# Kernel optimization log

Measured on AMD Instinct MI355X. Metric: run time of the kernel, lower is better.

The kernel has to match this reference:

```python
import jax, jax.numpy as jnp
import numpy as np

B, T, DE, DD, A, FN, FS = 32, 2000, 512, 1024, 128, 32, 16
TEMPERATURE = 1.0


def setup_inputs() -> dict:
    key = jax.random.key(0)
    ks = jax.random.split(key, 10)
    input_enc = jax.random.normal(ks[0], (B, T, DE), dtype=jnp.float32)
    # lengths in [T//2, T] so no zero-length utterances
    enc_lengths = jax.random.randint(ks[1], (B,), T // 2, T + 1, dtype=jnp.int32)
    input_dec = jax.random.normal(ks[2], (B, DD), dtype=jnp.float32)
    # prev_att: previous-step attention weights (masked, normalized)
    prev_att = jax.random.uniform(ks[3], (B, T), dtype=jnp.float32)
    pad = jnp.arange(T)[None, :] >= enc_lengths[:, None]
    prev_att = jnp.where(pad, 0.0, prev_att)
    prev_att = prev_att / jnp.sum(prev_att, axis=1, keepdims=True)
    # parameters
    conv_w = jax.random.normal(ks[4], (FN, 1, 2 * FS + 1), dtype=jnp.float32) * 0.1  # [out,in,k]
    enc_w = jax.random.normal(ks[5], (A, DE), dtype=jnp.float32) * 0.04
    dec_w = jax.random.normal(ks[6], (A, DD), dtype=jnp.float32) * 0.03
    att_w = jax.random.normal(ks[7], (A, FN), dtype=jnp.float32) * 0.17
    att_b = jnp.zeros((A,), dtype=jnp.float32)
    out_w = jax.random.normal(ks[8], (1, A), dtype=jnp.float32) * 0.09
    return dict(input_enc=input_enc, enc_lengths=enc_lengths, input_dec=input_dec,
                prev_att=prev_att, conv_w=conv_w, enc_w=enc_w, dec_w=dec_w,
                att_w=att_w, att_b=att_b, out_w=out_w)


def reference(input_enc, enc_lengths, input_dec, prev_att,
              conv_w, enc_w, dec_w, att_w, att_b, out_w):
    b, t, _ = input_enc.shape
    fs = (conv_w.shape[-1] - 1) // 2  # 'same' padding
    # padding mask: True at padded positions t >= length
    mask = jnp.arange(t)[None, :] >= enc_lengths[:, None]  # [B,T]
    # location features: Conv1d over prev attention, 1 -> FN channels, same length
    conv = jax.lax.conv_general_dilated(
        prev_att[:, None, :], conv_w, window_strides=(1,),
        padding=[(fs, fs)], dimension_numbers=("NCH", "OIH", "NCH"))  # [B,FN,T]
    loc_feat = conv.transpose(0, 2, 1)  # [B,T,FN]
    projected_att = loc_feat @ att_w.T + att_b        # [B,T,A]
    projected_enc = input_enc @ enc_w.T               # [B,T,A]
    projected_dec = (input_dec @ dec_w.T)[:, None, :]  # [B,1,A]
    score = jnp.squeeze(jnp.tanh(projected_att + projected_enc + projected_dec) @ out_w.T, -1)  # [B,T]
    score = jnp.where(mask, -jnp.inf, score)
    att_weight = jax.nn.softmax(TEMPERATURE * score, axis=1)  # [B,T]
    context = jnp.einsum("btd,bt->bd", input_enc, att_weight)  # [B,DE]
    return context, att_weight
```

## Files before the change

### kernel.cpp

```cpp
#include <hip/hip_runtime.h>
#include <hip/hip_bf16.h>
#include <math.h>

#define B_ 32
#define T_ 2000
#define DE_ 512
#define DD_ 1024
#define A_ 128
#define FN_ 32
#define FS_ 16
#define KW_ (2*FS_+1)

typedef __bf16 bf16x8 __attribute__((ext_vector_type(8)));
typedef __bf16 bf16x4 __attribute__((ext_vector_type(4)));
typedef float f32x4 __attribute__((ext_vector_type(4)));

#define BT 64
#define LSTR 40

__global__ __launch_bounds__(256) void cvt_kernel(
    const float* __restrict__ enc_w, const float* __restrict__ att_w,
    __bf16* __restrict__ enc_bf, __bf16* __restrict__ att_bf)
{
    int i = blockIdx.x * 256 + threadIdx.x;
    float4 v = ((const float4*)enc_w)[i];
    bf16x4 o;
    o[0] = (__bf16)v.x; o[1] = (__bf16)v.y; o[2] = (__bf16)v.z; o[3] = (__bf16)v.w;
    *(bf16x4*)(enc_bf + (size_t)i * 4) = o;
    if (i < (A_ * FN_) / 4) {
        float4 w = ((const float4*)att_w)[i];
        bf16x4 p;
        p[0] = (__bf16)w.x; p[1] = (__bf16)w.y; p[2] = (__bf16)w.z; p[3] = (__bf16)w.w;
        *(bf16x4*)(att_bf + (size_t)i * 4) = p;
    }
}

__global__ __launch_bounds__(256) void pdec_kernel(
    const float* __restrict__ input_dec, const float* __restrict__ dec_w,
    const float* __restrict__ att_b, float* __restrict__ pdec)
{
    int b  = blockIdx.y;
    int a0 = blockIdx.x * 32;
    int tid = threadIdx.x;
    int al = tid >> 3;
    int kg = tid & 7;
    int a  = a0 + al;
    const float4* w = (const float4*)(dec_w + (size_t)a * DD_);
    const float4* x = (const float4*)(input_dec + (size_t)b * DD_);
    float acc = 0.f;
    #pragma unroll 8
    for (int j = 0; j < 32; j++) {
        int i4 = kg + j * 8;
        float4 wv = w[i4], xv = x[i4];
        acc += wv.x * xv.x + wv.y * xv.y + wv.z * xv.z + wv.w * xv.w;
    }
    acc += __shfl_xor(acc, 1, 64);
    acc += __shfl_xor(acc, 2, 64);
    acc += __shfl_xor(acc, 4, 64);
    if (kg == 0) pdec[b * A_ + a] = acc + att_b[a];
}

__global__ __launch_bounds__(256, 4) void score_kernel(
    const float* __restrict__ input_enc, const __bf16* __restrict__ enc_bf,
    const float* __restrict__ prev_att,  const float* __restrict__ conv_w,
    const __bf16* __restrict__ att_bf,   const float* __restrict__ pdec,
    const float* __restrict__ out_w,     float* __restrict__ score)
{
    __shared__ float pa_s[BT + 2 * FS_];
    __shared__ float cw_s[KW_ * FN_];
    __shared__ __bf16 loc_s[BT * LSTR];

    const int tid = threadIdx.x;
    const int b  = blockIdx.y;
    const int t0 = blockIdx.x * BT;

    for (int j = tid; j < BT + 2 * FS_; j += 256) {
        int t = t0 - FS_ + j;
        pa_s[j] = (t >= 0 && t < T_) ? prev_att[b * T_ + t] : 0.f;
    }
    for (int idx = tid; idx < FN_ * KW_; idx += 256) {
        int f = idx / KW_, k = idx % KW_;
        cw_s[k * FN_ + f] = conv_w[idx];
    }
    __syncthreads();

    {
        int f = tid & 31, r0 = tid >> 5;
        for (int r = r0; r < BT; r += 8) {
            float acc = 0.f;
            #pragma unroll
            for (int k = 0; k < KW_; k++) acc += pa_s[r + k] * cw_s[k * FN_ + f];
            loc_s[r * LSTR + f] = (__bf16)acc;
        }
    }
    __syncthreads();

    const int lane = tid & 63;
    const int wv   = tid >> 6;
    const int col  = lane & 15;
    const int grp  = lane >> 4;
    const int rowb = wv * 16 + col;
    const int t_row = t0 + rowb;
    const int t_clamp = t_row < T_ ? t_row : T_ - 1;

    f32x4 acc[8];
    const f32x4 zero = (f32x4){0.f, 0.f, 0.f, 0.f};

    {
        bf16x8 afrag = *(const bf16x8*)(loc_s + rowb * LSTR + grp * 8);
        #pragma unroll
        for (int i = 0; i < 8; i++) {
            bf16x8 bfrag = *(const bf16x8*)(att_bf + (size_t)(i * 16 + col) * FN_ + grp * 8);
            acc[i] = __builtin_amdgcn_mfma_f32_16x16x32_bf16(afrag, bfrag, zero, 0, 0, 0);
        }
    }

    const float* arow = input_enc + ((size_t)(b * T_ + t_clamp)) * DE_ + grp * 8;
    const __bf16* bbase = enc_bf + (size_t)col * DE_ + grp * 8;
    #pragma unroll 2
    for (int kc = 0; kc < DE_; kc += 32) {
        float4 a0v = *(const float4*)(arow + kc);
        float4 a1v = *(const float4*)(arow + kc + 4);
        bf16x8 afrag;
        afrag[0] = (__bf16)a0v.x; afrag[1] = (__bf16)a0v.y;
        afrag[2] = (__bf16)a0v.z; afrag[3] = (__bf16)a0v.w;
        afrag[4] = (__bf16)a1v.x; afrag[5] = (__bf16)a1v.y;
        afrag[6] = (__bf16)a1v.z; afrag[7] = (__bf16)a1v.w;
        #pragma unroll
        for (int i = 0; i < 8; i++) {
            bf16x8 bfrag = *(const bf16x8*)(bbase + (size_t)i * 16 * DE_ + kc);
            acc[i] = __builtin_amdgcn_mfma_f32_16x16x32_bf16(afrag, bfrag, acc[i], 0, 0, 0);
        }
    }

    float s[4] = {0.f, 0.f, 0.f, 0.f};
    #pragma unroll
    for (int i = 0; i < 8; i++) {
        int a = i * 16 + col;
        float ow = out_w[a];
        float bias = pdec[b * A_ + a];
        #pragma unroll
        for (int r = 0; r < 4; r++) {
            float v = acc[i][r] + bias;
            v = fminf(fmaxf(v, -15.f), 15.f);
            float e = __expf(2.f * v);
            s[r] += ow * ((e - 1.f) / (e + 1.f));
        }
    }
    #pragma unroll
    for (int r = 0; r < 4; r++) {
        s[r] += __shfl_xor(s[r], 1, 64);
        s[r] += __shfl_xor(s[r], 2, 64);
        s[r] += __shfl_xor(s[r], 4, 64);
        s[r] += __shfl_xor(s[r], 8, 64);
    }
    if (col == 0) {
        #pragma unroll
        for (int r = 0; r < 4; r++) {
            int t = t0 + wv * 16 + grp * 4 + r;
            if (t < T_) score[b * T_ + t] = s[r];
        }
    }
}

__global__ __launch_bounds__(256) void softmax_kernel(
    const float* __restrict__ score, const int* __restrict__ lengths,
    float* __restrict__ att)
{
    int b = blockIdx.x;
    int tid = threadIdx.x;
    int len = lengths[b];
    __shared__ float redm[4], reds[4];

    float m = -1e30f;
    for (int t = tid; t < T_; t += 256)
        if (t < len) m = fmaxf(m, score[b * T_ + t]);
    #pragma unroll
    for (int off = 1; off < 64; off <<= 1) m = fmaxf(m, __shfl_xor(m, off, 64));
    if ((tid & 63) == 0) redm[tid >> 6] = m;
    __syncthreads();
    m = fmaxf(fmaxf(redm[0], redm[1]), fmaxf(redm[2], redm[3]));

    float sum = 0.f;
    for (int t = tid; t < T_; t += 256)
        if (t < len) sum += expf(score[b * T_ + t] - m);
    #pragma unroll
    for (int off = 1; off < 64; off <<= 1) sum += __shfl_xor(sum, off, 64);
    if ((tid & 63) == 0) reds[tid >> 6] = sum;
    __syncthreads();
    sum = reds[0] + reds[1] + reds[2] + reds[3];
    float inv = 1.f / sum;

    for (int t = tid; t < T_; t += 256) {
        float w = (t < len) ? expf(score[b * T_ + t] - m) * inv : 0.f;
        att[b * T_ + t] = w;
    }
}

#define CT 125
__global__ __launch_bounds__(256) void context_kernel(
    const float* __restrict__ enc, const float* __restrict__ att,
    const int* __restrict__ lengths, float* __restrict__ ctx)
{
    int b = blockIdx.y;
    int tstart = blockIdx.x * CT;
    int len = lengths[b];
    int tend = tstart + CT < len ? tstart + CT : len;
    __shared__ float w_s[CT];
    for (int j = threadIdx.x; j < CT; j += 256) w_s[j] = att[b * T_ + tstart + j];
    __syncthreads();
    if (tstart >= tend) return;

    int d0 = threadIdx.x * 2;
    const float* base = enc + ((size_t)(b * T_ + tstart)) * DE_ + d0;
    float ax = 0.f, ay = 0.f;
    int n = tend - tstart;
    #pragma unroll 4
    for (int t = 0; t < n; t++) {
        float w = w_s[t];
        float2 v = *(const float2*)(base + (size_t)t * DE_);
        ax += w * v.x;
        ay += w * v.y;
    }
    atomicAdd(&ctx[b * DE_ + d0], ax);
    atomicAdd(&ctx[b * DE_ + d0 + 1], ay);
}

extern "C" void kernel_launch(void* const* d_in, const int* in_sizes, int n_in,
                              void* d_out, int out_size, void* d_ws, size_t ws_size,
                              hipStream_t stream)
{
    const float* input_enc   = (const float*)d_in[0];
    const int*   enc_lengths = (const int*)d_in[1];
    const float* input_dec   = (const float*)d_in[2];
    const float* prev_att    = (const float*)d_in[3];
    const float* conv_w      = (const float*)d_in[4];
    const float* enc_w       = (const float*)d_in[5];
    const float* dec_w       = (const float*)d_in[6];
    const float* att_w       = (const float*)d_in[7];
    const float* att_b       = (const float*)d_in[8];
    const float* out_w       = (const float*)d_in[9];

    float* out = (float*)d_out;
    char* ws = (char*)d_ws;
    float*  pdec   = (float*)ws;
    float*  score  = (float*)(ws + 16384);
    __bf16* enc_bf = (__bf16*)(ws + 16384 + 256000);
    __bf16* att_bf = (__bf16*)(ws + 16384 + 256000 + 131072);

    hipMemsetAsync(d_out, 0, (size_t)B_ * DE_ * sizeof(float), stream);

    cvt_kernel<<<(A_ * DE_) / 4 / 256, 256, 0, stream>>>(enc_w, att_w, enc_bf, att_bf);

    dim3 pgrid(4, B_);
    pdec_kernel<<<pgrid, 256, 0, stream>>>(input_dec, dec_w, att_b, pdec);

    dim3 sgrid((T_ + BT - 1) / BT, B_);
    score_kernel<<<sgrid, 256, 0, stream>>>(input_enc, enc_bf, prev_att, conv_w,
                                            att_bf, pdec, out_w, score);

    softmax_kernel<<<B_, 256, 0, stream>>>(score, enc_lengths, out + B_ * DE_);

    dim3 cgrid(16, B_);
    context_kernel<<<cgrid, 256, 0, stream>>>(input_enc, out + B_ * DE_, enc_lengths, out);
}
```

Baseline: 276.6 us.

## Stage enc weights in LDS, merge prep kernels, fuse softmax normalize into context

Merges the weight-conversion and decoder-projection kernels into one launch and drops the memset by zeroing the context output inside the softmax-stats kernel. The score kernel now stages bf16 encoder-weight tiles into swizzled shared memory through global_load_lds, instead of each wave reading them from global. Softmax now only computes the max and inverse sum; the context kernel computes the normalized weights, writes them out, and uses float4 loads over more, smaller chunks. This removes launches and a full pass over the scores, at the cost of extra barriers in the score loop and the reuse of the pdec buffer for the softmax stats.

```diff
diff --git a/kernel.cpp b/kernel.cpp
--- a/kernel.cpp
+++ b/kernel.cpp
@@ -18,46 +18,53 @@
 #define BT 64
 #define LSTR 40
 
-__global__ __launch_bounds__(256) void cvt_kernel(
+__device__ __forceinline__ void load_lds16(const void* g, void* l) {
+    __builtin_amdgcn_global_load_lds(
+        (const __attribute__((address_space(1))) unsigned int*)g,
+        (__attribute__((address_space(3))) unsigned int*)l, 16, 0, 0);
+}
+
+__global__ __launch_bounds__(256) void prep_kernel(
     const float* __restrict__ enc_w, const float* __restrict__ att_w,
-    __bf16* __restrict__ enc_bf, __bf16* __restrict__ att_bf)
-{
-    int i = blockIdx.x * 256 + threadIdx.x;
-    float4 v = ((const float4*)enc_w)[i];
-    bf16x4 o;
-    o[0] = (__bf16)v.x; o[1] = (__bf16)v.y; o[2] = (__bf16)v.z; o[3] = (__bf16)v.w;
-    *(bf16x4*)(enc_bf + (size_t)i * 4) = o;
-    if (i < (A_ * FN_) / 4) {
-        float4 w = ((const float4*)att_w)[i];
-        bf16x4 p;
-        p[0] = (__bf16)w.x; p[1] = (__bf16)w.y; p[2] = (__bf16)w.z; p[3] = (__bf16)w.w;
-        *(bf16x4*)(att_bf + (size_t)i * 4) = p;
-    }
-}
-
-__global__ __launch_bounds__(256) void pdec_kernel(
     const float* __restrict__ input_dec, const float* __restrict__ dec_w,
-    const float* __restrict__ att_b, float* __restrict__ pdec)
-{
-    int b  = blockIdx.y;
-    int a0 = blockIdx.x * 32;
-    int tid = threadIdx.x;
-    int al = tid >> 3;
-    int kg = tid & 7;
-    int a  = a0 + al;
-    const float4* w = (const float4*)(dec_w + (size_t)a * DD_);
-    const float4* x = (const float4*)(input_dec + (size_t)b * DD_);
-    float acc = 0.f;
-    #pragma unroll 8
-    for (int j = 0; j < 32; j++) {
-        int i4 = kg + j * 8;
-        float4 wv = w[i4], xv = x[i4];
-        acc += wv.x * xv.x + wv.y * xv.y + wv.z * xv.z + wv.w * xv.w;
-    }
-    acc += __shfl_xor(acc, 1, 64);
-    acc += __shfl_xor(acc, 2, 64);
-    acc += __shfl_xor(acc, 4, 64);
-    if (kg == 0) pdec[b * A_ + a] = acc + att_b[a];
+    const float* __restrict__ att_b,
+    __bf16* __restrict__ enc_bf, __bf16* __restrict__ att_bf,
+    float* __restrict__ pdec)
+{
+    int bx = blockIdx.x, tid = threadIdx.x;
+    if (bx < 64) {
+        int i = bx * 256 + tid;
+        float4 v = ((const float4*)enc_w)[i];
+        bf16x4 o;
+        o[0] = (__bf16)v.x; o[1] = (__bf16)v.y; o[2] = (__bf16)v.z; o[3] = (__bf16)v.w;
+        *(bf16x4*)(enc_bf + (size_t)i * 4) = o;
+        if (i < (A_ * FN_) / 4) {
+            float4 w = ((const float4*)att_w)[i];
+            bf16x4 p;
+            p[0] = (__bf16)w.x; p[1] = (__bf16)w.y; p[2] = (__bf16)w.z; p[3] = (__bf16)w.w;
+            *(bf16x4*)(att_bf + (size_t)i * 4) = p;
+        }
+    } else {
+        int pb = bx - 64;
+        int b  = pb >> 2;
+        int a0 = (pb & 3) * 32;
+        int al = tid >> 3;
+        int kg = tid & 7;
+        int a  = a0 + al;
+        const float4* w = (const float4*)(dec_w + (size_t)a * DD_);
+        const float4* x = (const float4*)(input_dec + (size_t)b * DD_);
+        float acc = 0.f;
+        #pragma unroll 8
+        for (int j = 0; j < 32; j++) {
+            int i4 = kg + j * 8;
+            float4 wv = w[i4], xv = x[i4];
+            acc += wv.x * xv.x + wv.y * xv.y + wv.z * xv.z + wv.w * xv.w;
+        }
+        acc += __shfl_xor(acc, 1, 64);
+        acc += __shfl_xor(acc, 2, 64);
+        acc += __shfl_xor(acc, 4, 64);
+        if (kg == 0) pdec[b * A_ + a] = acc + att_b[a];
+    }
 }
 
 __global__ __launch_bounds__(256, 4) void score_kernel(
@@ -66,9 +73,10 @@
     const __bf16* __restrict__ att_bf,   const float* __restrict__ pdec,
     const float* __restrict__ out_w,     float* __restrict__ score)
 {
+    __shared__ __align__(16) char Bt[16384];
     __shared__ float pa_s[BT + 2 * FS_];
     __shared__ float cw_s[KW_ * FN_];
-    __shared__ __bf16 loc_s[BT * LSTR];
+    __shared__ __align__(16) __bf16 loc_s[BT * LSTR];
 
     const int tid = threadIdx.x;
     const int b  = blockIdx.y;
@@ -102,6 +110,7 @@
     const int rowb = wv * 16 + col;
     const int t_row = t0 + rowb;
     const int t_clamp = t_row < T_ ? t_row : T_ - 1;
+    const int sw = (col & 7);
 
     f32x4 acc[8];
     const f32x4 zero = (f32x4){0.f, 0.f, 0.f, 0.f};
@@ -116,21 +125,43 @@
     }
 
     const float* arow = input_enc + ((size_t)(b * T_ + t_clamp)) * DE_ + grp * 8;
-    const __bf16* bbase = enc_bf + (size_t)col * DE_ + grp * 8;
-    #pragma unroll 2
-    for (int kc = 0; kc < DE_; kc += 32) {
-        float4 a0v = *(const float4*)(arow + kc);
-        float4 a1v = *(const float4*)(arow + kc + 4);
-        bf16x8 afrag;
-        afrag[0] = (__bf16)a0v.x; afrag[1] = (__bf16)a0v.y;
-        afrag[2] = (__bf16)a0v.z; afrag[3] = (__bf16)a0v.w;
-        afrag[4] = (__bf16)a1v.x; afrag[5] = (__bf16)a1v.y;
-        afrag[6] = (__bf16)a1v.z; afrag[7] = (__bf16)a1v.w;
+
+    for (int kc = 0; kc < DE_; kc += 64) {
+        #pragma unroll
+        for (int j = 0; j < 4; j++) {
+            int s  = j * 256 + tid;
+            int r  = s >> 3;
+            int cp = s & 7;
+            int c  = cp ^ (r & 7);
+            load_lds16(enc_bf + (size_t)r * DE_ + kc + c * 8,
+                       Bt + j * 4096 + wv * 1024);
+        }
+        float4 a00 = *(const float4*)(arow + kc);
+        float4 a01 = *(const float4*)(arow + kc + 4);
+        float4 a10 = *(const float4*)(arow + kc + 32);
+        float4 a11 = *(const float4*)(arow + kc + 36);
+        __syncthreads();
+
+        bf16x8 af;
+        af[0] = (__bf16)a00.x; af[1] = (__bf16)a00.y;
+        af[2] = (__bf16)a00.z; af[3] = (__bf16)a00.w;
+        af[4] = (__bf16)a01.x; af[5] = (__bf16)a01.y;
+        af[6] = (__bf16)a01.z; af[7] = (__bf16)a01.w;
         #pragma unroll
         for (int i = 0; i < 8; i++) {
-            bf16x8 bfrag = *(const bf16x8*)(bbase + (size_t)i * 16 * DE_ + kc);
-            acc[i] = __builtin_amdgcn_mfma_f32_16x16x32_bf16(afrag, bfrag, acc[i], 0, 0, 0);
-        }
+            bf16x8 bfrag = *(const bf16x8*)(Bt + (i * 16 + col) * 128 + ((grp ^ sw) * 16));
+            acc[i] = __builtin_amdgcn_mfma_f32_16x16x32_bf16(af, bfrag, acc[i], 0, 0, 0);
+        }
+        af[0] = (__bf16)a10.x; af[1] = (__bf16)a10.y;
+        af[2] = (__bf16)a10.z; af[3] = (__bf16)a10.w;
+        af[4] = (__bf16)a11.x; af[5] = (__bf16)a11.y;
+        af[6] = (__bf16)a11.z; af[7] = (__bf16)a11.w;
+        #pragma unroll
+        for (int i = 0; i < 8; i++) {
+            bf16x8 bfrag = *(const bf16x8*)(Bt + (i * 16 + col) * 128 + (((4 + grp) ^ sw) * 16));
+            acc[i] = __builtin_amdgcn_mfma_f32_16x16x32_bf16(af, bfrag, acc[i], 0, 0, 0);
+        }
+        __syncthreads();
     }
 
     float s[4] = {0.f, 0.f, 0.f, 0.f};
@@ -163,12 +194,14 @@
     }
 }
 
-__global__ __launch_bounds__(256) void softmax_kernel(
+__global__ __launch_bounds__(256) void smax_kernel(
     const float* __restrict__ score, const int* __restrict__ lengths,
-    float* __restrict__ att)
+    float* __restrict__ minv, float* __restrict__ ctx)
 {
     int b = blockIdx.x;
     int tid = threadIdx.x;
+    if (tid < 128)
+        *(float4*)(ctx + b * DE_ + tid * 4) = make_float4(0.f, 0.f, 0.f, 0.f);
     int len = lengths[b];
     __shared__ float redm[4], reds[4];
 
@@ -183,47 +216,56 @@
 
     float sum = 0.f;
     for (int t = tid; t < T_; t += 256)
-        if (t < len) sum += expf(score[b * T_ + t] - m);
+        if (t < len) sum += __expf(score[b * T_ + t] - m);
     #pragma unroll
     for (int off = 1; off < 64; off <<= 1) sum += __shfl_xor(sum, off, 64);
     if ((tid & 63) == 0) reds[tid >> 6] = sum;
     __syncthreads();
-    sum = reds[0] + reds[1] + reds[2] + reds[3];
-    float inv = 1.f / sum;
-
-    for (int t = tid; t < T_; t += 256) {
-        float w = (t < len) ? expf(score[b * T_ + t] - m) * inv : 0.f;
-        att[b * T_ + t] = w;
-    }
-}
-
-#define CT 125
+    if (tid == 0) {
+        sum = reds[0] + reds[1] + reds[2] + reds[3];
+        minv[2 * b] = m;
+        minv[2 * b + 1] = 1.f / sum;
+    }
+}
+
+#define NCH 32
+#define CCH 63
 __global__ __launch_bounds__(256) void context_kernel(
-    const float* __restrict__ enc, const float* __restrict__ att,
-    const int* __restrict__ lengths, float* __restrict__ ctx)
+    const float* __restrict__ enc, const float* __restrict__ score,
+    const float* __restrict__ minv, const int* __restrict__ lengths,
+    float* __restrict__ att, float* __restrict__ ctx)
 {
     int b = blockIdx.y;
-    int tstart = blockIdx.x * CT;
+    int tstart = blockIdx.x * CCH;
     int len = lengths[b];
-    int tend = tstart + CT < len ? tstart + CT : len;
-    __shared__ float w_s[CT];
-    for (int j = threadIdx.x; j < CT; j += 256) w_s[j] = att[b * T_ + tstart + j];
-    __syncthreads();
+    float m = minv[2 * b], inv = minv[2 * b + 1];
+    __shared__ float w_s[CCH];
+    for (int j = threadIdx.x; j < CCH; j += 256) {
+        int t = tstart + j;
+        float w = 0.f;
+        if (t < len) w = __expf(score[b * T_ + t] - m) * inv;
+        if (t < T_) att[b * T_ + t] = w;
+        w_s[j] = w;
+    }
+    __syncthreads();
+
+    int tend = tstart + CCH < len ? tstart + CCH : len;
     if (tstart >= tend) return;
-
-    int d0 = threadIdx.x * 2;
+    int n = tend - tstart;
+    int half = threadIdx.x >> 7;
+    int d0 = (threadIdx.x & 127) * 4;
     const float* base = enc + ((size_t)(b * T_ + tstart)) * DE_ + d0;
-    float ax = 0.f, ay = 0.f;
-    int n = tend - tstart;
+    float ax = 0.f, ay = 0.f, az = 0.f, aw = 0.f;
     #pragma unroll 4
-    for (int t = 0; t < n; t++) {
+    for (int t = half; t < n; t += 2) {
         float w = w_s[t];
-        float2 v = *(const float2*)(base + (size_t)t * DE_);
-        ax += w * v.x;
-        ay += w * v.y;
-    }
-    atomicAdd(&ctx[b * DE_ + d0], ax);
+        float4 v = *(const float4*)(base + (size_t)t * DE_);
+        ax += w * v.x; ay += w * v.y; az += w * v.z; aw += w * v.w;
+    }
+    atomicAdd(&ctx[b * DE_ + d0 + 0], ax);
     atomicAdd(&ctx[b * DE_ + d0 + 1], ay);
+    atomicAdd(&ctx[b * DE_ + d0 + 2], az);
+    atomicAdd(&ctx[b * DE_ + d0 + 3], aw);
 }
 
 extern "C" void kernel_launch(void* const* d_in, const int* in_sizes, int n_in,
@@ -247,20 +289,18 @@
     float*  score  = (float*)(ws + 16384);
     __bf16* enc_bf = (__bf16*)(ws + 16384 + 256000);
     __bf16* att_bf = (__bf16*)(ws + 16384 + 256000 + 131072);
-
-    hipMemsetAsync(d_out, 0, (size_t)B_ * DE_ * sizeof(float), stream);
-
-    cvt_kernel<<<(A_ * DE_) / 4 / 256, 256, 0, stream>>>(enc_w, att_w, enc_bf, att_bf);
-
-    dim3 pgrid(4, B_);
-    pdec_kernel<<<pgrid, 256, 0, stream>>>(input_dec, dec_w, att_b, pdec);
+    float*  minv   = pdec;
+
+    prep_kernel<<<192, 256, 0, stream>>>(enc_w, att_w, input_dec, dec_w, att_b,
+                                         enc_bf, att_bf, pdec);
 
     dim3 sgrid((T_ + BT - 1) / BT, B_);
     score_kernel<<<sgrid, 256, 0, stream>>>(input_enc, enc_bf, prev_att, conv_w,
                                             att_bf, pdec, out_w, score);
 
-    softmax_kernel<<<B_, 256, 0, stream>>>(score, enc_lengths, out + B_ * DE_);
-
-    dim3 cgrid(16, B_);
-    context_kernel<<<cgrid, 256, 0, stream>>>(input_enc, out + B_ * DE_, enc_lengths, out);
-}
+    smax_kernel<<<B_, 256, 0, stream>>>(score, enc_lengths, minv, out);
+
+    dim3 cgrid(NCH, B_);
+    context_kernel<<<cgrid, 256, 0, stream>>>(input_enc, score, minv, enc_lengths,
+                                              out + B_ * DE_, out);
+}
```

Measured after the change: 245.8 us. -11.1%, faster.
